# Performance work log

Measured on AMD Instinct MI355X. Metric: run time of the kernel, lower is better.

## Reference

```python
import jax, jax.numpy as jnp
import numpy as np

N = 100000      # nodes
E = 1200000     # edges (avg degree ~12)
D_IN = 64
D_OUT = 64


def setup_inputs() -> dict:
    key = jax.random.key(0)
    k1, k2, k3, k4 = jax.random.split(key, 4)
    x = jax.random.normal(k1, (N, D_IN), dtype=jnp.float32)
    # learned params (glorot-ish init)
    W = jax.random.normal(k2, (D_IN, D_OUT), dtype=jnp.float32) / np.sqrt(D_IN).astype(np.float32)
    b = jnp.zeros((D_OUT,), dtype=jnp.float32)
    src = jax.random.randint(k3, (E,), 0, N, dtype=jnp.int32)
    dst = jax.random.randint(k4, (E,), 0, N, dtype=jnp.int32)
    return {"x": x, "W": W, "b": b, "src": src, "dst": dst}


def reference(x, W, b, src, dst):
    # GCN layer: h = relu( D^-1/2 A D^-1/2 (x @ W) + b ), dropout=0 (eval)
    ones = jnp.ones(src.shape[0], dtype=x.dtype)
    deg_out = jax.ops.segment_sum(ones, src, num_segments=N)   # out-degree of source nodes
    deg_in = jax.ops.segment_sum(ones, dst, num_segments=N)    # in-degree of dest nodes
    norm_src = jax.lax.rsqrt(jnp.maximum(deg_out, 1.0))
    norm_dst = jax.lax.rsqrt(jnp.maximum(deg_in, 1.0))

    h = x @ W                                                  # [N, D_OUT] dense transform
    msg = h[src] * norm_src[src][:, None]                      # [E, D_OUT] gathered, pre-normalized messages
    agg = jax.ops.segment_sum(msg, dst, num_segments=N)        # [N, D_OUT] sparse aggregation
    out = agg * norm_dst[:, None] + b
    return jax.nn.relu(out)
```

## Files before the change

### kernel.cpp

```cpp
#include <hip/hip_runtime.h>
#include <hip/hip_bf16.h>

#define N_NODES 100000
#define N_EDGES 1200000
#define DCH 64

#define FB 256
#define NT 1024
#define EPB 4688
#define GW_TOT (FB * NT / 64)

#define HALF_BINS 50000
#define HALF_WORDS 12500

#define BNODES 128
#define KBUK ((N_NODES + BNODES - 1) / BNODES)
#define CAPE 3008

#define NT2 512

#define OFF_DEG      0
#define OFF_GCUR     100096
#define OFF_FLAG     103296
#define OFF_ESORT    103424
#define OFF_HS       9512704

__device__ __forceinline__ float load_f(const void* p, int i, int f32) {
    if (f32) return ((const float*)p)[i];
    return __bfloat162float(((const __hip_bfloat16*)p)[i]);
}

__device__ __forceinline__ unsigned short f2bf_bits(float f) {
    __hip_bfloat16 h = __float2bfloat16(f);
    return __builtin_bit_cast(unsigned short, h);
}

__global__ __launch_bounds__(NT, 4)
void fused_kernel(const int* __restrict__ src,
                  const int* __restrict__ dst,
                  const void* __restrict__ x,
                  const void* __restrict__ W,
                  unsigned int* __restrict__ deg_packed,
                  int* __restrict__ gcur,
                  unsigned int* __restrict__ esort,
                  int* __restrict__ flag,
                  __hip_bfloat16* __restrict__ hs) {
    __shared__ unsigned int h[HALF_WORDS];
    int tid = threadIdx.x;
    int bid = blockIdx.x;

    int* sn = (int*)h;
    if (tid == 0) sn[0] = 0;
    __syncthreads();
    if (tid < 256) {
        const unsigned short* u = (const unsigned short*)x;
        int c = 0;
        for (int i = tid * 16; i < tid * 16 + 16; ++i) {
            unsigned short v = u[2 * i];
            int e = (v >> 7) & 0xFF;
            if (e >= 141) c++;
        }
        if (c) atomicAdd(sn, c);
    }
    __syncthreads();
    int f32 = sn[0] > 256;
    if (bid == 0 && tid == 0) *flag = f32;
    __syncthreads();

    {
        float* wt = (float*)h;
        for (int i = tid; i < DCH * DCH; i += NT) {
            int kk = i >> 6, cc = i & 63;
            wt[cc * 68 + kk] = load_f(W, i, f32);
        }
        __syncthreads();

        int lane = tid & 63;
        const float4* wrow = (const float4*)(wt + lane * 68);
        float4 wq0 = wrow[0],  wq1 = wrow[1],  wq2 = wrow[2],  wq3 = wrow[3];
        float4 wq4 = wrow[4],  wq5 = wrow[5],  wq6 = wrow[6],  wq7 = wrow[7];
        float4 wq8 = wrow[8],  wq9 = wrow[9],  wq10 = wrow[10], wq11 = wrow[11];
        float4 wq12 = wrow[12], wq13 = wrow[13], wq14 = wrow[14], wq15 = wrow[15];

        int gw = (bid << 4) + (tid >> 6);
#define RLA(i) __int_as_float(__builtin_amdgcn_readlane(xiA, (i)))
#define RLB(i) __int_as_float(__builtin_amdgcn_readlane(xiB, (i)))
#define GRP(j, V) \
    a0 = fmaf(RLA(4*(j)+0), (V).x, a0); a1 = fmaf(RLA(4*(j)+1), (V).y, a1); \
    a2 = fmaf(RLA(4*(j)+2), (V).z, a2); a3 = fmaf(RLA(4*(j)+3), (V).w, a3); \
    c0 = fmaf(RLB(4*(j)+0), (V).x, c0); c1 = fmaf(RLB(4*(j)+1), (V).y, c1); \
    c2 = fmaf(RLB(4*(j)+2), (V).z, c2); c3 = fmaf(RLB(4*(j)+3), (V).w, c3);

        for (int node = gw; node < N_NODES; node += 2 * GW_TOT) {
            int nodeB = node + GW_TOT;
            int hasB = nodeB < N_NODES;
            float xvA = load_f(x, node * DCH + lane, f32);
            float xvB = hasB ? load_f(x, nodeB * DCH + lane, f32) : 0.0f;
            int xiA = __float_as_int(xvA);
            int xiB = __float_as_int(xvB);
            float a0 = 0.f, a1 = 0.f, a2 = 0.f, a3 = 0.f;
            float c0 = 0.f, c1 = 0.f, c2 = 0.f, c3 = 0.f;
            GRP(0, wq0)   GRP(1, wq1)   GRP(2, wq2)   GRP(3, wq3)
            GRP(4, wq4)   GRP(5, wq5)   GRP(6, wq6)   GRP(7, wq7)
            GRP(8, wq8)   GRP(9, wq9)   GRP(10, wq10) GRP(11, wq11)
            GRP(12, wq12) GRP(13, wq13) GRP(14, wq14) GRP(15, wq15)
            hs[node * DCH + lane] = __float2bfloat16((a0 + a1) + (a2 + a3));
            if (hasB)
                hs[nodeB * DCH + lane] = __float2bfloat16((c0 + c1) + (c2 + c3));
        }
#undef RLA
#undef RLB
#undef GRP
    }
    __syncthreads();

    int e0 = bid * EPB;
    int eend = e0 + EPB; if (eend > N_EDGES) eend = N_EDGES;
    int npair = (eend - e0) >> 1;
    const int2* src2 = (const int2*)(src + e0);
    const int2* dst2 = (const int2*)(dst + e0);

    for (int half = 0; half < 2; ++half) {
        for (int w = tid; w < HALF_WORDS; w += NT) h[w] = 0;
        __syncthreads();
        int lo = half * HALF_BINS;
        for (int p = tid; p < npair; p += NT) {
            int2 sp = src2[p];
            int n0 = sp.x - lo, n1 = sp.y - lo;
            if ((unsigned)n0 < (unsigned)HALF_BINS)
                atomicAdd(&h[n0 >> 2], 1u << ((n0 & 3) * 8));
            if ((unsigned)n1 < (unsigned)HALF_BINS)
                atomicAdd(&h[n1 >> 2], 1u << ((n1 & 3) * 8));
        }
        __syncthreads();
        unsigned int* dp = deg_packed + half * HALF_WORDS;
        for (int w = tid; w < HALF_WORDS; w += NT) {
            unsigned int v = h[w];
            if (v) atomicAdd(&dp[w], v);
        }
        __syncthreads();
    }

    {
        int* cnt  = (int*)h;
        int* base = cnt + KBUK;
        int* cur  = base + KBUK;
        for (int i = tid; i < KBUK; i += NT) { cnt[i] = 0; cur[i] = 0; }
        __syncthreads();
        for (int p = tid; p < npair; p += NT) {
            int2 dp = dst2[p];
            atomicAdd(&cnt[dp.x >> 7], 1);
            atomicAdd(&cnt[dp.y >> 7], 1);
        }
        __syncthreads();
        for (int i = tid; i < KBUK; i += NT)
            base[i] = atomicAdd(&gcur[i], cnt[i]);
        __syncthreads();
        for (int p = tid; p < npair; p += NT) {
            int2 sp = src2[p];
            int2 dp = dst2[p];
            int b0 = dp.x >> 7, b1 = dp.y >> 7;
            int pos0 = base[b0] + atomicAdd(&cur[b0], 1);
            if (pos0 < CAPE)
                esort[b0 * CAPE + pos0] =
                    (unsigned int)sp.x | ((unsigned int)(dp.x & 127) << 24);
            int pos1 = base[b1] + atomicAdd(&cur[b1], 1);
            if (pos1 < CAPE)
                esort[b1 * CAPE + pos1] =
                    (unsigned int)sp.y | ((unsigned int)(dp.y & 127) << 24);
        }
    }
}

__global__ __launch_bounds__(NT2, 6)
void sortgather_kernel(const __hip_bfloat16* __restrict__ hs,
                       const unsigned int* __restrict__ esort,
                       const int* __restrict__ gcur,
                       const unsigned int* __restrict__ deg_packed,
                       const void* __restrict__ b,
                       const int* __restrict__ flag,
                       void* __restrict__ out) {
    __shared__ unsigned int ebuf[CAPE];
    __shared__ int cnt[BNODES];
    __shared__ int loc[BNODES];
    __shared__ int sc[BNODES];
    __shared__ int cur[BNODES];
    __shared__ float tab[256];
    int k = blockIdx.x, tid = threadIdx.x;
    int bbase = k * CAPE;
    int m = gcur[k];
    if (m > CAPE) m = CAPE;

    if (tid < BNODES) { cnt[tid] = 0; cur[tid] = 0; }
    if (tid < 256) tab[tid] = rsqrtf(fmaxf((float)tid, 1.0f));
    __syncthreads();
    for (int e = tid; e < m; e += NT2)
        atomicAdd(&cnt[esort[bbase + e] >> 24], 1);
    __syncthreads();
    int v = 0;
    if (tid < BNODES) { v = cnt[tid]; sc[tid] = v; }
    __syncthreads();
    for (int off = 1; off < BNODES; off <<= 1) {
        int add = 0;
        if (tid < BNODES && tid >= off) add = sc[tid - off];
        __syncthreads();
        if (tid < BNODES) sc[tid] += add;
        __syncthreads();
    }
    if (tid < BNODES) loc[tid] = sc[tid] - v;
    __syncthreads();
    for (int e = tid; e < m; e += NT2) {
        unsigned int w = esort[bbase + e];
        int r = w >> 24;
        unsigned int s = w & 0xFFFFFFu;
        unsigned int dw = deg_packed[s >> 2];
        unsigned int degb = (dw >> ((s & 3) * 8)) & 0xFFu;
        int pos = loc[r] + atomicAdd(&cur[r], 1);
        ebuf[pos] = s | (degb << 24);
    }
    __syncthreads();

    int f32 = *flag;
    int lane = tid & 63, wv = tid >> 6;
    int q = lane >> 4;
    int cg = lane & 15;
    const unsigned short* hsu = (const unsigned short*)hs;
    float b0 = load_f(b, cg * 4 + 0, f32);
    float b1 = load_f(b, cg * 4 + 1, f32);
    float b2 = load_f(b, cg * 4 + 2, f32);
    float b3 = load_f(b, cg * 4 + 3, f32);
    int nlo = k * BNODES;
    for (int base = wv; base < BNODES; base += 16) {
        int tA = base, tB = base + 8;
        int nodeA = nlo + tA, nodeB = nlo + tB;
        int begA = loc[tA], degA = cnt[tA];
        int begB = loc[tB], degB = cnt[tB];
        float4 aA0 = {0.f,0.f,0.f,0.f}, aA1 = {0.f,0.f,0.f,0.f};
        float4 aB0 = {0.f,0.f,0.f,0.f}, aB1 = {0.f,0.f,0.f,0.f};
        int dmax = degA > degB ? degA : degB;
        for (int j0 = 0; j0 < dmax; j0 += 8) {
            int i0 = j0 + q, i1 = j0 + 4 + q;
            unsigned int wA0 = ebuf[(i0 < degA) ? (begA + i0) : 0];
            unsigned int wA1 = ebuf[(i1 < degA) ? (begA + i1) : 0];
            unsigned int wB0 = ebuf[(i0 < degB) ? (begB + i0) : 0];
            unsigned int wB1 = ebuf[(i1 < degB) ? (begB + i1) : 0];
            unsigned int sA0 = wA0 & 0xFFFFFFu, sA1 = wA1 & 0xFFFFFFu;
            unsigned int sB0 = wB0 & 0xFFFFFFu, sB1 = wB1 & 0xFFFFFFu;
            float fA0 = tab[wA0 >> 24], fA1 = tab[wA1 >> 24];
            float fB0 = tab[wB0 >> 24], fB1 = tab[wB1 >> 24];
            uint2 uA0 = ((const uint2*)(hsu + sA0 * DCH))[cg];
            uint2 uA1 = ((const uint2*)(hsu + sA1 * DCH))[cg];
            uint2 uB0 = ((const uint2*)(hsu + sB0 * DCH))[cg];
            uint2 uB1 = ((const uint2*)(hsu + sB1 * DCH))[cg];
            if (i0 < degA) {
                aA0.x = fmaf(__uint_as_float(uA0.x << 16),        fA0, aA0.x);
                aA0.y = fmaf(__uint_as_float(uA0.x & 0xFFFF0000u), fA0, aA0.y);
                aA0.z = fmaf(__uint_as_float(uA0.y << 16),        fA0, aA0.z);
                aA0.w = fmaf(__uint_as_float(uA0.y & 0xFFFF0000u), fA0, aA0.w);
            }
            if (i1 < degA) {
                aA1.x = fmaf(__uint_as_float(uA1.x << 16),        fA1, aA1.x);
                aA1.y = fmaf(__uint_as_float(uA1.x & 0xFFFF0000u), fA1, aA1.y);
                aA1.z = fmaf(__uint_as_float(uA1.y << 16),        fA1, aA1.z);
                aA1.w = fmaf(__uint_as_float(uA1.y & 0xFFFF0000u), fA1, aA1.w);
            }
            if (i0 < degB) {
                aB0.x = fmaf(__uint_as_float(uB0.x << 16),        fB0, aB0.x);
                aB0.y = fmaf(__uint_as_float(uB0.x & 0xFFFF0000u), fB0, aB0.y);
                aB0.z = fmaf(__uint_as_float(uB0.y << 16),        fB0, aB0.z);
                aB0.w = fmaf(__uint_as_float(uB0.y & 0xFFFF0000u), fB0, aB0.w);
            }
            if (i1 < degB) {
                aB1.x = fmaf(__uint_as_float(uB1.x << 16),        fB1, aB1.x);
                aB1.y = fmaf(__uint_as_float(uB1.x & 0xFFFF0000u), fB1, aB1.y);
                aB1.z = fmaf(__uint_as_float(uB1.y << 16),        fB1, aB1.z);
                aB1.w = fmaf(__uint_as_float(uB1.y & 0xFFFF0000u), fB1, aB1.w);
            }
        }
        float4 oA, oB;
        oA.x = aA0.x + aA1.x; oA.y = aA0.y + aA1.y;
        oA.z = aA0.z + aA1.z; oA.w = aA0.w + aA1.w;
        oB.x = aB0.x + aB1.x; oB.y = aB0.y + aB1.y;
        oB.z = aB0.z + aB1.z; oB.w = aB0.w + aB1.w;
        oA.x += __shfl_xor(oA.x, 16); oA.y += __shfl_xor(oA.y, 16);
        oA.z += __shfl_xor(oA.z, 16); oA.w += __shfl_xor(oA.w, 16);
        oA.x += __shfl_xor(oA.x, 32); oA.y += __shfl_xor(oA.y, 32);
        oA.z += __shfl_xor(oA.z, 32); oA.w += __shfl_xor(oA.w, 32);
        oB.x += __shfl_xor(oB.x, 16); oB.y += __shfl_xor(oB.y, 16);
        oB.z += __shfl_xor(oB.z, 16); oB.w += __shfl_xor(oB.w, 16);
        oB.x += __shfl_xor(oB.x, 32); oB.y += __shfl_xor(oB.y, 32);
        oB.z += __shfl_xor(oB.z, 32); oB.w += __shfl_xor(oB.w, 32);
        int myNode = (lane < 16) ? nodeA : nodeB;
        int myDeg  = (lane < 16) ? degA : degB;
        float4 o   = (lane < 16) ? oA : oB;
        if (lane < 32 && myNode < N_NODES) {
            float nrm = rsqrtf(fmaxf((float)myDeg, 1.0f));
            o.x = fmaxf(o.x * nrm + b0, 0.0f);
            o.y = fmaxf(o.y * nrm + b1, 0.0f);
            o.z = fmaxf(o.z * nrm + b2, 0.0f);
            o.w = fmaxf(o.w * nrm + b3, 0.0f);
            if (f32) {
                ((float4*)out)[myNode * 16 + cg] = o;
            } else {
                ushort4 s;
                s.x = f2bf_bits(o.x);
                s.y = f2bf_bits(o.y);
                s.z = f2bf_bits(o.z);
                s.w = f2bf_bits(o.w);
                ((ushort4*)out)[myNode * 16 + cg] = s;
            }
        }
    }
}

extern "C" void kernel_launch(void* const* d_in, const int* in_sizes, int n_in,
                              void* d_out, int out_size, void* d_ws, size_t ws_size,
                              hipStream_t stream) {
    const void* x   = d_in[0];
    const void* W   = d_in[1];
    const void* b   = d_in[2];
    const int*  src = (const int*)d_in[3];
    const int*  dst = (const int*)d_in[4];

    char* ws = (char*)d_ws;
    unsigned int* deg_packed = (unsigned int*)(ws + OFF_DEG);
    int* gcur     = (int*)(ws + OFF_GCUR);
    int* flag     = (int*)(ws + OFF_FLAG);
    unsigned int* esort = (unsigned int*)(ws + OFF_ESORT);
    __hip_bfloat16* hs  = (__hip_bfloat16*)(ws + OFF_HS);

    (void)hipMemsetAsync(ws, 0, OFF_FLAG + 4, stream);

    fused_kernel<<<FB, NT, 0, stream>>>(
        src, dst, x, W, deg_packed, gcur, esort, flag, hs);

    sortgather_kernel<<<KBUK, NT2, 0, stream>>>(
        hs, esort, gcur, deg_packed, b, flag, d_out);
}
```

Measured before the change: 173.6 us.

## Split degree histogram halves across blocks and deepen gather unroll

```diff
diff --git a/kernel.cpp b/kernel.cpp
--- a/kernel.cpp
+++ b/kernel.cpp
@@ -8,6 +8,8 @@
 #define FB 256
 #define NT 1024
 #define EPB 4688
+#define PPB 2344
+#define HPAIRS 4688
 #define GW_TOT (FB * NT / 64)
 
 #define HALF_BINS 50000
@@ -77,19 +79,29 @@
 
         int lane = tid & 63;
         const float4* wrow = (const float4*)(wt + lane * 68);
-        float4 wq0 = wrow[0],  wq1 = wrow[1],  wq2 = wrow[2],  wq3 = wrow[3];
-        float4 wq4 = wrow[4],  wq5 = wrow[5],  wq6 = wrow[6],  wq7 = wrow[7];
-        float4 wq8 = wrow[8],  wq9 = wrow[9],  wq10 = wrow[10], wq11 = wrow[11];
-        float4 wq12 = wrow[12], wq13 = wrow[13], wq14 = wrow[14], wq15 = wrow[15];
+        float wr[DCH];
+#pragma unroll
+        for (int kq = 0; kq < 16; ++kq) {
+            float4 t = wrow[kq];
+            wr[4 * kq + 0] = t.x; wr[4 * kq + 1] = t.y;
+            wr[4 * kq + 2] = t.z; wr[4 * kq + 3] = t.w;
+        }
+#pragma unroll
+        for (int kk = 0; kk < DCH; ++kk)
+            asm volatile("" : "+v"(wr[kk]));
 
         int gw = (bid << 4) + (tid >> 6);
 #define RLA(i) __int_as_float(__builtin_amdgcn_readlane(xiA, (i)))
 #define RLB(i) __int_as_float(__builtin_amdgcn_readlane(xiB, (i)))
-#define GRP(j, V) \
-    a0 = fmaf(RLA(4*(j)+0), (V).x, a0); a1 = fmaf(RLA(4*(j)+1), (V).y, a1); \
-    a2 = fmaf(RLA(4*(j)+2), (V).z, a2); a3 = fmaf(RLA(4*(j)+3), (V).w, a3); \
-    c0 = fmaf(RLB(4*(j)+0), (V).x, c0); c1 = fmaf(RLB(4*(j)+1), (V).y, c1); \
-    c2 = fmaf(RLB(4*(j)+2), (V).z, c2); c3 = fmaf(RLB(4*(j)+3), (V).w, c3);
+#define GRP(j) \
+    a0 = fmaf(RLA(4*(j)+0), wr[4*(j)+0], a0); \
+    a1 = fmaf(RLA(4*(j)+1), wr[4*(j)+1], a1); \
+    a2 = fmaf(RLA(4*(j)+2), wr[4*(j)+2], a2); \
+    a3 = fmaf(RLA(4*(j)+3), wr[4*(j)+3], a3); \
+    c0 = fmaf(RLB(4*(j)+0), wr[4*(j)+0], c0); \
+    c1 = fmaf(RLB(4*(j)+1), wr[4*(j)+1], c1); \
+    c2 = fmaf(RLB(4*(j)+2), wr[4*(j)+2], c2); \
+    c3 = fmaf(RLB(4*(j)+3), wr[4*(j)+3], c3);
 
         for (int node = gw; node < N_NODES; node += 2 * GW_TOT) {
             int nodeB = node + GW_TOT;
@@ -100,10 +112,10 @@
             int xiB = __float_as_int(xvB);
             float a0 = 0.f, a1 = 0.f, a2 = 0.f, a3 = 0.f;
             float c0 = 0.f, c1 = 0.f, c2 = 0.f, c3 = 0.f;
-            GRP(0, wq0)   GRP(1, wq1)   GRP(2, wq2)   GRP(3, wq3)
-            GRP(4, wq4)   GRP(5, wq5)   GRP(6, wq6)   GRP(7, wq7)
-            GRP(8, wq8)   GRP(9, wq9)   GRP(10, wq10) GRP(11, wq11)
-            GRP(12, wq12) GRP(13, wq13) GRP(14, wq14) GRP(15, wq15)
+            GRP(0)  GRP(1)  GRP(2)  GRP(3)
+            GRP(4)  GRP(5)  GRP(6)  GRP(7)
+            GRP(8)  GRP(9)  GRP(10) GRP(11)
+            GRP(12) GRP(13) GRP(14) GRP(15)
             hs[node * DCH + lane] = __float2bfloat16((a0 + a1) + (a2 + a3));
             if (hasB)
                 hs[nodeB * DCH + lane] = __float2bfloat16((c0 + c1) + (c2 + c3));
@@ -114,18 +126,18 @@
     }
     __syncthreads();
 
-    int e0 = bid * EPB;
-    int eend = e0 + EPB; if (eend > N_EDGES) eend = N_EDGES;
-    int npair = (eend - e0) >> 1;
-    const int2* src2 = (const int2*)(src + e0);
-    const int2* dst2 = (const int2*)(dst + e0);
-
-    for (int half = 0; half < 2; ++half) {
+    {
+        int half = bid & 1;
+        int j = bid >> 1;
+        int p0 = j * HPAIRS;
+        int p1 = p0 + HPAIRS;
+        if (p1 > N_EDGES / 2) p1 = N_EDGES / 2;
+        const int2* s2 = (const int2*)src;
         for (int w = tid; w < HALF_WORDS; w += NT) h[w] = 0;
         __syncthreads();
         int lo = half * HALF_BINS;
-        for (int p = tid; p < npair; p += NT) {
-            int2 sp = src2[p];
+        for (int p = p0 + tid; p < p1; p += NT) {
+            int2 sp = s2[p];
             int n0 = sp.x - lo, n1 = sp.y - lo;
             if ((unsigned)n0 < (unsigned)HALF_BINS)
                 atomicAdd(&h[n0 >> 2], 1u << ((n0 & 3) * 8));
@@ -142,6 +154,12 @@
     }
 
     {
+        int e0 = bid * EPB;
+        int eend = e0 + EPB; if (eend > N_EDGES) eend = N_EDGES;
+        int npair = (eend - e0) >> 1;
+        const int2* src2 = (const int2*)(src + e0);
+        const int2* dst2 = (const int2*)(dst + e0);
+
         int* cnt  = (int*)h;
         int* base = cnt + KBUK;
         int* cur  = base + KBUK;
@@ -230,58 +248,63 @@
     float b2 = load_f(b, cg * 4 + 2, f32);
     float b3 = load_f(b, cg * 4 + 3, f32);
     int nlo = k * BNODES;
+
+#define ACC(ACCV, U, F) \
+    (ACCV).x = fmaf(__uint_as_float((U).x << 16),         (F), (ACCV).x); \
+    (ACCV).y = fmaf(__uint_as_float((U).x & 0xFFFF0000u), (F), (ACCV).y); \
+    (ACCV).z = fmaf(__uint_as_float((U).y << 16),         (F), (ACCV).z); \
+    (ACCV).w = fmaf(__uint_as_float((U).y & 0xFFFF0000u), (F), (ACCV).w);
+
     for (int base = wv; base < BNODES; base += 16) {
         int tA = base, tB = base + 8;
         int nodeA = nlo + tA, nodeB = nlo + tB;
         int begA = loc[tA], degA = cnt[tA];
         int begB = loc[tB], degB = cnt[tB];
         float4 aA0 = {0.f,0.f,0.f,0.f}, aA1 = {0.f,0.f,0.f,0.f};
+        float4 aA2 = {0.f,0.f,0.f,0.f}, aA3 = {0.f,0.f,0.f,0.f};
         float4 aB0 = {0.f,0.f,0.f,0.f}, aB1 = {0.f,0.f,0.f,0.f};
+        float4 aB2 = {0.f,0.f,0.f,0.f}, aB3 = {0.f,0.f,0.f,0.f};
         int dmax = degA > degB ? degA : degB;
-        for (int j0 = 0; j0 < dmax; j0 += 8) {
-            int i0 = j0 + q, i1 = j0 + 4 + q;
+        for (int j0 = 0; j0 < dmax; j0 += 16) {
+            int i0 = j0 + q, i1 = j0 + 4 + q, i2 = j0 + 8 + q, i3 = j0 + 12 + q;
             unsigned int wA0 = ebuf[(i0 < degA) ? (begA + i0) : 0];
             unsigned int wA1 = ebuf[(i1 < degA) ? (begA + i1) : 0];
+            unsigned int wA2 = ebuf[(i2 < degA) ? (begA + i2) : 0];
+            unsigned int wA3 = ebuf[(i3 < degA) ? (begA + i3) : 0];
             unsigned int wB0 = ebuf[(i0 < degB) ? (begB + i0) : 0];
             unsigned int wB1 = ebuf[(i1 < degB) ? (begB + i1) : 0];
-            unsigned int sA0 = wA0 & 0xFFFFFFu, sA1 = wA1 & 0xFFFFFFu;
-            unsigned int sB0 = wB0 & 0xFFFFFFu, sB1 = wB1 & 0xFFFFFFu;
+            unsigned int wB2 = ebuf[(i2 < degB) ? (begB + i2) : 0];
+            unsigned int wB3 = ebuf[(i3 < degB) ? (begB + i3) : 0];
+            uint2 uA0 = ((const uint2*)(hsu + (wA0 & 0xFFFFFFu) * DCH))[cg];
+            uint2 uA1 = ((const uint2*)(hsu + (wA1 & 0xFFFFFFu) * DCH))[cg];
+            uint2 uA2 = ((const uint2*)(hsu + (wA2 & 0xFFFFFFu) * DCH))[cg];
+            uint2 uA3 = ((const uint2*)(hsu + (wA3 & 0xFFFFFFu) * DCH))[cg];
+            uint2 uB0 = ((const uint2*)(hsu + (wB0 & 0xFFFFFFu) * DCH))[cg];
+            uint2 uB1 = ((const uint2*)(hsu + (wB1 & 0xFFFFFFu) * DCH))[cg];
+            uint2 uB2 = ((const uint2*)(hsu + (wB2 & 0xFFFFFFu) * DCH))[cg];
+            uint2 uB3 = ((const uint2*)(hsu + (wB3 & 0xFFFFFFu) * DCH))[cg];
             float fA0 = tab[wA0 >> 24], fA1 = tab[wA1 >> 24];
+            float fA2 = tab[wA2 >> 24], fA3 = tab[wA3 >> 24];
             float fB0 = tab[wB0 >> 24], fB1 = tab[wB1 >> 24];
-            uint2 uA0 = ((const uint2*)(hsu + sA0 * DCH))[cg];
-            uint2 uA1 = ((const uint2*)(hsu + sA1 * DCH))[cg];
-            uint2 uB0 = ((const uint2*)(hsu + sB0 * DCH))[cg];
-            uint2 uB1 = ((const uint2*)(hsu + sB1 * DCH))[cg];
-            if (i0 < degA) {
-                aA0.x = fmaf(__uint_as_float(uA0.x << 16),        fA0, aA0.x);
-                aA0.y = fmaf(__uint_as_float(uA0.x & 0xFFFF0000u), fA0, aA0.y);
-                aA0.z = fmaf(__uint_as_float(uA0.y << 16),        fA0, aA0.z);
-                aA0.w = fmaf(__uint_as_float(uA0.y & 0xFFFF0000u), fA0, aA0.w);
-            }
-            if (i1 < degA) {
-                aA1.x = fmaf(__uint_as_float(uA1.x << 16),        fA1, aA1.x);
-                aA1.y = fmaf(__uint_as_float(uA1.x & 0xFFFF0000u), fA1, aA1.y);
-                aA1.z = fmaf(__uint_as_float(uA1.y << 16),        fA1, aA1.z);
-                aA1.w = fmaf(__uint_as_float(uA1.y & 0xFFFF0000u), fA1, aA1.w);
-            }
-            if (i0 < degB) {
-                aB0.x = fmaf(__uint_as_float(uB0.x << 16),        fB0, aB0.x);
-                aB0.y = fmaf(__uint_as_float(uB0.x & 0xFFFF0000u), fB0, aB0.y);
-                aB0.z = fmaf(__uint_as_float(uB0.y << 16),        fB0, aB0.z);
-                aB0.w = fmaf(__uint_as_float(uB0.y & 0xFFFF0000u), fB0, aB0.w);
-            }
-            if (i1 < degB) {
-                aB1.x = fmaf(__uint_as_float(uB1.x << 16),        fB1, aB1.x);
-                aB1.y = fmaf(__uint_as_float(uB1.x & 0xFFFF0000u), fB1, aB1.y);
-                aB1.z = fmaf(__uint_as_float(uB1.y << 16),        fB1, aB1.z);
-                aB1.w = fmaf(__uint_as_float(uB1.y & 0xFFFF0000u), fB1, aB1.w);
-            }
+            float fB2 = tab[wB2 >> 24], fB3 = tab[wB3 >> 24];
+            if (i0 < degA) { ACC(aA0, uA0, fA0) }
+            if (i1 < degA) { ACC(aA1, uA1, fA1) }
+            if (i2 < degA) { ACC(aA2, uA2, fA2) }
+            if (i3 < degA) { ACC(aA3, uA3, fA3) }
+            if (i0 < degB) { ACC(aB0, uB0, fB0) }
+            if (i1 < degB) { ACC(aB1, uB1, fB1) }
+            if (i2 < degB) { ACC(aB2, uB2, fB2) }
+            if (i3 < degB) { ACC(aB3, uB3, fB3) }
         }
         float4 oA, oB;
-        oA.x = aA0.x + aA1.x; oA.y = aA0.y + aA1.y;
-        oA.z = aA0.z + aA1.z; oA.w = aA0.w + aA1.w;
-        oB.x = aB0.x + aB1.x; oB.y = aB0.y + aB1.y;
-        oB.z = aB0.z + aB1.z; oB.w = aB0.w + aB1.w;
+        oA.x = (aA0.x + aA1.x) + (aA2.x + aA3.x);
+        oA.y = (aA0.y + aA1.y) + (aA2.y + aA3.y);
+        oA.z = (aA0.z + aA1.z) + (aA2.z + aA3.z);
+        oA.w = (aA0.w + aA1.w) + (aA2.w + aA3.w);
+        oB.x = (aB0.x + aB1.x) + (aB2.x + aB3.x);
+        oB.y = (aB0.y + aB1.y) + (aB2.y + aB3.y);
+        oB.z = (aB0.z + aB1.z) + (aB2.z + aB3.z);
+        oB.w = (aB0.w + aB1.w) + (aB2.w + aB3.w);
         oA.x += __shfl_xor(oA.x, 16); oA.y += __shfl_xor(oA.y, 16);
         oA.z += __shfl_xor(oA.z, 16); oA.w += __shfl_xor(oA.w, 16);
         oA.x += __shfl_xor(oA.x, 32); oA.y += __shfl_xor(oA.y, 32);
@@ -311,6 +334,7 @@
             }
         }
     }
+#undef ACC
 }
 
 extern "C" void kernel_launch(void* const* d_in, const int* in_sizes, int n_in,
```

New measurement: 173.3 us. No clear change (-0.2%).
